# Performance work log

Hardware: AMD Instinct MI355X
Metric: run time of the kernel (lower is better)

The kernel has to match this reference:

```python
import jax, jax.numpy as jnp
import numpy as np

B, S, E, H = 2, 4096, 512, 8
DK = E // H


def setup_inputs() -> dict:
    k = jax.random.key(0)
    ks = jax.random.split(k, 11)
    sc = 0.02
    return {
        "query": jax.random.normal(ks[0], (B, S, E), jnp.float32),
        "key_in": jax.random.normal(ks[1], (B, S, E), jnp.float32),
        "value": jax.random.normal(ks[2], (B, S, E), jnp.float32),
        "Wq": jax.random.normal(ks[3], (E, E), jnp.float32) * sc,
        "bq": jax.random.normal(ks[4], (E,), jnp.float32) * sc,
        "Wk": jax.random.normal(ks[5], (E, E), jnp.float32) * sc,
        "bk": jax.random.normal(ks[6], (E,), jnp.float32) * sc,
        "Wv": jax.random.normal(ks[7], (E, E), jnp.float32) * sc,
        "bv": jax.random.normal(ks[8], (E,), jnp.float32) * sc,
        "Wo": jax.random.normal(ks[9], (E, E), jnp.float32) * sc,
        "bo": jax.random.normal(ks[10], (E,), jnp.float32) * sc,
    }


def reference(query, key_in, value, Wq, bq, Wk, bk, Wv, bv, Wo, bo):
    b, s, _ = query.shape
    # Linear projections
    q = query @ Wq + bq
    k = key_in @ Wk + bk
    v = value @ Wv + bv
    # [b, s, H, dk] -> [b, H, s, dk]
    q = q.reshape(b, s, H, DK).transpose(0, 2, 1, 3)
    k = k.reshape(b, s, H, DK).transpose(0, 2, 1, 3)
    v = v.reshape(b, s, H, DK).transpose(0, 2, 1, 3)
    # NOTE: source bug — softmax over UNSCALED scores (1/sqrt scaling in the
    # original is applied to a dead variable after softmax). Reproduce faithfully.
    scores = jnp.einsum("bhqd,bhkd->bhqk", q, k)  # [b,H,s,s] — O(N^2) materialized
    weights = jax.nn.softmax(scores.astype(jnp.float32), axis=-1)
    attn = jnp.einsum("bhqk,bhkd->bhqd", weights, v)
    # [b,H,s,dk] -> [b,s,E]
    concat = attn.transpose(0, 2, 1, 3).reshape(b, s, E)
    return concat @ Wo + bo
```

## Files before the change

kernel.cpp:

```cpp
#include <hip/hip_runtime.h>
#include <hip/hip_bf16.h>

#define B_  2
#define S_  4096
#define E_  512
#define H_  8
#define DK_ 64
#define M_  8192

typedef float f32x4  __attribute__((ext_vector_type(4)));
typedef float f32x16 __attribute__((ext_vector_type(16)));
typedef short s16x8  __attribute__((ext_vector_type(8)));
typedef short s16x4  __attribute__((ext_vector_type(4)));

static __device__ __forceinline__ short f2bf(float x) {
  __hip_bfloat16 h = __float2bfloat16(x);
  return __builtin_bit_cast(short, h);
}

static __device__ __forceinline__ f32x4 mfma32(s16x8 a, s16x8 b, f32x4 c) {
  return __builtin_amdgcn_mfma_f32_16x16x32_bf16(a, b, c, 0, 0, 0);
}

static __device__ __forceinline__ f32x16 mfma3232(s16x8 a, s16x8 b, f32x16 c) {
  return __builtin_amdgcn_mfma_f32_32x32x16_bf16(a, b, c, 0, 0, 0);
}

static __device__ __forceinline__ float fastexp2(float x) {
#if __has_builtin(__builtin_amdgcn_exp2f)
  return __builtin_amdgcn_exp2f(x);
#else
  return __expf(x * 0.69314718056f);
#endif
}

static __device__ __forceinline__ void gload_lds16(const void* g, void* l) {
  __builtin_amdgcn_global_load_lds(
      (const __attribute__((address_space(1))) unsigned int*)g,
      (__attribute__((address_space(3))) unsigned int*)l, 16, 0, 0);
}

__global__ __launch_bounds__(256) void conv_wT_all(
    const float* __restrict__ Wq, const float* __restrict__ Wk,
    const float* __restrict__ Wv, const float* __restrict__ Wo,
    short* __restrict__ Wt) {
  const float* W = (blockIdx.y == 0) ? Wq
                   : ((blockIdx.y == 1) ? Wk : ((blockIdx.y == 2) ? Wv : Wo));
  short* o = Wt + (size_t)blockIdx.y * (E_ * E_);
  int idx = blockIdx.x * 256 + threadIdx.x;
  int j = idx >> 9, k = idx & 511;
  o[idx] = f2bf(W[(size_t)k * E_ + j]);
}

static __device__ __forceinline__ void gemm_core_512(
    const short* __restrict__ A, const short* __restrict__ Bt,
    short* As, short* Bs, int tm, int tn, f32x4 acc[4][4]) {
  const int tid = threadIdx.x;
  const int wave = tid >> 6, lane = tid & 63;
  const int c = lane & 15, g = lane >> 4;
  int fOff[2];
#pragma unroll
  for (int r = 0; r < 2; ++r) {
    const int f = wave * 2 + r;
    fOff[r] = ((f >> 2) * 64 + (f & 3) * 16 + c) * 512 + g * 8;
  }
  auto stg = [&](int p, int b) {
#pragma unroll
    for (int r = 0; r < 2; ++r) {
      const int f = wave * 2 + r;
      gload_lds16(A + (size_t)tm * 512 + p * 32 + fOff[r],
                  (char*)As + b * 8192 + f * 1024);
      gload_lds16(Bt + (size_t)tn * 512 + p * 32 + fOff[r],
                  (char*)Bs + b * 8192 + f * 1024);
    }
  };
  stg(0, 0);
  __syncthreads();
  for (int p = 0; p < 16; ++p) {
    if (p + 1 < 16) stg(p + 1, (p + 1) & 1);
    const short* Ac = As + (p & 1) * 4096;
    const short* Bc = Bs + (p & 1) * 4096;
    s16x8 af[4], bfr[4];
#pragma unroll
    for (int i = 0; i < 4; ++i)
      af[i] = *(const s16x8*)(Ac + ((wave >> 1) * 4 + i) * 512 + lane * 8);
#pragma unroll
    for (int j = 0; j < 4; ++j)
      bfr[j] = *(const s16x8*)(Bc + ((wave & 1) * 4 + j) * 512 + lane * 8);
#pragma unroll
    for (int i = 0; i < 4; ++i)
#pragma unroll
      for (int j = 0; j < 4; ++j)
        acc[i][j] = mfma32(af[i], bfr[j], acc[i][j]);
    __syncthreads();
  }
}

static __device__ __forceinline__ void gemm_core_f32A(
    const float* __restrict__ A, const short* __restrict__ Bt,
    short* As, short* Bs, int tm, int tn, f32x4 acc[4][4]) {
  const int tid = threadIdx.x;
  const int wave = tid >> 6, lane = tid & 63;
  const int c = lane & 15, g = lane >> 4;
  int fOff[2];
#pragma unroll
  for (int r = 0; r < 2; ++r) {
    const int f = wave * 2 + r;
    fOff[r] = ((f >> 2) * 64 + (f & 3) * 16 + c) * 512 + g * 8;
  }
  auto stgB = [&](int p, int b) {
#pragma unroll
    for (int r = 0; r < 2; ++r)
      gload_lds16(Bt + (size_t)tn * 512 + p * 32 + fOff[r],
                  (char*)Bs + b * 8192 + (wave * 2 + r) * 1024);
  };
  float4 a0[2], a1[2];
  auto ldA = [&](int p) {
#pragma unroll
    for (int r = 0; r < 2; ++r) {
      const float* ap = A + (size_t)tm * 512 + p * 32 + fOff[r];
      a0[r] = *(const float4*)ap;
      a1[r] = *(const float4*)(ap + 4);
    }
  };
  auto wrA = [&](int b) {
#pragma unroll
    for (int r = 0; r < 2; ++r) {
      s16x8 w;
      w[0] = f2bf(a0[r].x); w[1] = f2bf(a0[r].y);
      w[2] = f2bf(a0[r].z); w[3] = f2bf(a0[r].w);
      w[4] = f2bf(a1[r].x); w[5] = f2bf(a1[r].y);
      w[6] = f2bf(a1[r].z); w[7] = f2bf(a1[r].w);
      *(s16x8*)((char*)As + b * 8192 + (wave * 2 + r) * 1024 + lane * 16) = w;
    }
  };
  ldA(0); stgB(0, 0); wrA(0);
  __syncthreads();
  for (int p = 0; p < 16; ++p) {
    if (p + 1 < 16) { ldA(p + 1); stgB(p + 1, (p + 1) & 1); }
    const short* Ac = As + (p & 1) * 4096;
    const short* Bc = Bs + (p & 1) * 4096;
    s16x8 af[4], bfr[4];
#pragma unroll
    for (int i = 0; i < 4; ++i)
      af[i] = *(const s16x8*)(Ac + ((wave >> 1) * 4 + i) * 512 + lane * 8);
#pragma unroll
    for (int j = 0; j < 4; ++j)
      bfr[j] = *(const s16x8*)(Bc + ((wave & 1) * 4 + j) * 512 + lane * 8);
#pragma unroll
    for (int i = 0; i < 4; ++i)
#pragma unroll
      for (int j = 0; j < 4; ++j)
        acc[i][j] = mfma32(af[i], bfr[j], acc[i][j]);
    if (p + 1 < 16) wrA((p + 1) & 1);
    __syncthreads();
  }
}

__global__ __launch_bounds__(256) void gemm_qkv(
    const float* __restrict__ Xq, const float* __restrict__ Xk,
    const float* __restrict__ Xv, const short* __restrict__ Wt,
    const float* __restrict__ bq, const float* __restrict__ bk,
    const float* __restrict__ bv,
    short* __restrict__ Qo, short* __restrict__ Ko, short* __restrict__ Vto) {
  __shared__ __align__(16) short As[2 * 4096];
  __shared__ __align__(16) short Bs[2 * 4096];
  const int z = blockIdx.z;
  const float* A = (z == 0) ? Xq : ((z == 1) ? Xk : Xv);
  const short* Bt = Wt + z * (E_ * E_);
  const float* bias = (z == 0) ? bq : ((z == 1) ? bk : bv);
  const int tm = blockIdx.x * 128, tn = blockIdx.y * 128;
  f32x4 acc[4][4] = {};
  gemm_core_f32A(A, Bt, As, Bs, tm, tn, acc);

  const int tid = threadIdx.x;
  const int wave = tid >> 6, lane = tid & 63;
  const int wm = (wave >> 1) * 64, wn = (wave & 1) * 64;
  const int c = lane & 15, g = lane >> 4;
#pragma unroll
  for (int i = 0; i < 4; ++i) {
#pragma unroll
    for (int j = 0; j < 4; ++j) {
      const int gc = tn + wn + j * 16 + c;
      const float bb = bias[gc];
      const int h = gc >> 6, dk = gc & 63;
      if (z == 2) {
        const int gr0 = tm + wm + i * 16 + g * 4;
        const int b = gr0 >> 12, s0 = gr0 & 4095;
        s16x4 v4;
#pragma unroll
        for (int r = 0; r < 4; ++r) v4[r] = f2bf(acc[i][j][r] + bb);
        *(s16x4*)&Vto[(size_t)((b * H_ + h) * DK_ + dk) * S_ + s0] = v4;
      } else {
#pragma unroll
        for (int r = 0; r < 4; ++r) {
          const int gr = tm + wm + i * 16 + g * 4 + r;
          const int b = gr >> 12, s = gr & 4095;
          float v = acc[i][j][r] + bb;
          if (z == 0) v *= 1.44269504f;
          const short hv = f2bf(v);
          if (z == 1)
            Ko[(size_t)((b * H_ + h) * S_ + s) * DK_ + dk] = hv;
          else
            Qo[(size_t)((b * H_ + h) * S_ + s) * DK_ + dk] = hv;
        }
      }
    }
  }
}

__global__ __launch_bounds__(256) void gemm_out(
    const short* __restrict__ AO, const short* __restrict__ Wot,
    const float* __restrict__ bo, float* __restrict__ out) {
  __shared__ __align__(16) short As[2 * 4096];
  __shared__ __align__(16) short Bs[2 * 4096];
  const int tm = blockIdx.x * 128, tn = blockIdx.y * 128;
  f32x4 acc[4][4] = {};
  gemm_core_512(AO, Wot, As, Bs, tm, tn, acc);

  const int tid = threadIdx.x;
  const int wave = tid >> 6, lane = tid & 63;
  const int wm = (wave >> 1) * 64, wn = (wave & 1) * 64;
  const int c = lane & 15, g = lane >> 4;
#pragma unroll
  for (int i = 0; i < 4; ++i) {
#pragma unroll
    for (int j = 0; j < 4; ++j) {
      const int gc = tn + wn + j * 16 + c;
      const float bb = bo[gc];
#pragma unroll
      for (int r = 0; r < 4; ++r) {
        const int gr = tm + wm + i * 16 + g * 4 + r;
        out[(size_t)gr * E_ + gc] = acc[i][j][r] + bb;
      }
    }
  }
}

__global__ __launch_bounds__(512, 2) void attn_fwd(
    const short* __restrict__ Q, const short* __restrict__ K,
    const short* __restrict__ Vt, short* __restrict__ O) {
  __shared__ __align__(16) char lds[98304];
  const int tid = threadIdx.x;
  const int wave = tid >> 6, lane = tid & 63;
  const int g = wave >> 1, kh = wave & 1;
  const int qi = lane & 31, hi = lane >> 5;
  const int bh = blockIdx.y;
  const int b = bh >> 3, h = bh & 7;
  const int q0 = blockIdx.x * 256 + g * 64;
  const short* Qp = Q + (size_t)bh * S_ * DK_;
  const short* Kp = K + (size_t)bh * S_ * DK_;
  const short* Vp = Vt + (size_t)bh * DK_ * S_;

  s16x8 qfL[4], qfH[4];
#pragma unroll
  for (int s = 0; s < 4; ++s) {
    qfL[s] = *(const s16x8*)(Qp + (size_t)(q0 + qi) * DK_ + s * 16 + hi * 8);
    qfH[s] = *(const s16x8*)(Qp + (size_t)(q0 + 32 + qi) * DK_ + s * 16 + hi * 8);
  }

  f32x16 o00 = {}, o01 = {}, o10 = {}, o11 = {};
  float lsL = 0.f, lsH = 0.f;

  int kOff, vOff;
  {
    const int j = wave;
    const int row = (j >> 2) * 32 + qi;
    const int srow = (row & 32) | ((row & 8) << 1) | ((row & 4) << 1) |
                     ((row & 16) >> 2) | (row & 3);
    kOff = srow * DK_ + (j & 3) * 16 + hi * 8;
    vOff = ((j >> 2) * 32 + qi) * S_ + ((j >> 1) & 1) * 32 +
           (j & 1) * 16 + hi * 8;
  }

  auto stage = [&](int kt) {
    gload_lds16(Kp + (size_t)kt * 64 * DK_ + kOff,
                lds + (kt % 6) * 8192 + wave * 1024);
    gload_lds16(Vp + (size_t)kt * 64 + vOff,
                lds + 49152 + (kt % 6) * 8192 + wave * 1024);
  };

  auto bar4 = [&]() {
    asm volatile("s_waitcnt vmcnt(4) lgkmcnt(0)" ::: "memory");
    __builtin_amdgcn_s_barrier();
  };
  auto bar0 = [&]() {
    asm volatile("s_waitcnt vmcnt(0) lgkmcnt(0)" ::: "memory");
    __builtin_amdgcn_s_barrier();
  };

  const int lbK = kh * 4096 + (lane << 4);

  auto qk = [&](int t, f32x16& sL, f32x16& sH) {
    const char* Kc = lds + (t % 6) * 8192 + lbK;
    f32x16 a = {}, c = {};
    __builtin_amdgcn_s_setprio(1);
#pragma unroll
    for (int s = 0; s < 4; ++s) {
      s16x8 ka = *(const s16x8*)(Kc + s * 1024);
      a = mfma3232(ka, qfL[s], a);
      c = mfma3232(ka, qfH[s], c);
    }
    __builtin_amdgcn_s_setprio(0);
    sL = a; sH = c;
  };

  auto softpv = [&](const f32x16& sL, const f32x16& sH, int t) {
    const char* Vc = lds + 49152 + (t % 6) * 8192 + kh * 2048 + (lane << 4);
    float pL[16], pH[16];
#pragma unroll
    for (int r = 0; r < 16; ++r) { pL[r] = fastexp2(sL[r]); pH[r] = fastexp2(sH[r]); }
    float aL = 0.f, aH = 0.f;
#pragma unroll
    for (int r = 0; r < 16; ++r) { aL += pL[r]; aH += pH[r]; }
    lsL += aL; lsH += aH;
    s16x8 pbL[2], pbH[2];
#pragma unroll
    for (int ks = 0; ks < 2; ++ks)
#pragma unroll
      for (int j = 0; j < 8; ++j) {
        const int r = (j & 3) | (ks << 2) | ((j >> 2) << 3);
        pbL[ks][j] = f2bf(pL[r]);
        pbH[ks][j] = f2bf(pH[r]);
      }
    __builtin_amdgcn_s_setprio(1);
#pragma unroll
    for (int ks = 0; ks < 2; ++ks) {
      s16x8 va0 = *(const s16x8*)(Vc + ks * 1024);
      s16x8 va1 = *(const s16x8*)(Vc + 4096 + ks * 1024);
      o00 = mfma3232(va0, pbL[ks], o00);
      o01 = mfma3232(va0, pbH[ks], o01);
      o10 = mfma3232(va1, pbL[ks], o10);
      o11 = mfma3232(va1, pbH[ks], o11);
    }
    __builtin_amdgcn_s_setprio(0);
  };

  const int NT = S_ / 64;
  f32x16 sA0, sA1, sB0, sB1;

  stage(0); stage(1); stage(2); stage(3);
  bar4();

  for (int t = 0; t < NT; t += 2) {
    if (t + 4 < NT) { stage(t + 4); stage(t + 5); bar4(); } else bar0();
    qk(t, sA0, sA1);
    qk(t + 1, sB0, sB1);
    softpv(sA0, sA1, t);
    softpv(sB0, sB1, t + 1);
  }

  lsL += __shfl_xor(lsL, 32);
  lsH += __shfl_xor(lsH, 32);

  float* mrg = (float*)lds;
  const int mi = (g * 64 + lane) * 36;
  __syncthreads();
  if (kh) {
#pragma unroll
    for (int r = 0; r < 4; ++r) {
      *(f32x4*)(mrg + mi + r * 4) =
          f32x4{o00[r * 4], o00[r * 4 + 1], o00[r * 4 + 2], o00[r * 4 + 3]};
      *(f32x4*)(mrg + mi + 16 + r * 4) =
          f32x4{o01[r * 4], o01[r * 4 + 1], o01[r * 4 + 2], o01[r * 4 + 3]};
    }
    mrg[mi + 32] = lsL;
    mrg[mi + 33] = lsH;
  }
  __syncthreads();
  float rlL = 0.f, rlH = 0.f;
  if (!kh) {
#pragma unroll
    for (int r = 0; r < 16; ++r) {
      o00[r] += mrg[mi + r];
      o01[r] += mrg[mi + 16 + r];
    }
    rlL = 1.f / (lsL + mrg[mi + 32]);
    rlH = 1.f / (lsH + mrg[mi + 33]);
  }
  __syncthreads();
  if (kh) {
#pragma unroll
    for (int r = 0; r < 4; ++r) {
      *(f32x4*)(mrg + mi + r * 4) =
          f32x4{o10[r * 4], o10[r * 4 + 1], o10[r * 4 + 2], o10[r * 4 + 3]};
      *(f32x4*)(mrg + mi + 16 + r * 4) =
          f32x4{o11[r * 4], o11[r * 4 + 1], o11[r * 4 + 2], o11[r * 4 + 3]};
    }
  }
  __syncthreads();
  if (!kh) {
#pragma unroll
    for (int r = 0; r < 16; ++r) {
      o10[r] += mrg[mi + r];
      o11[r] += mrg[mi + 16 + r];
    }
    short* OpL = O + ((size_t)(b * S_ + q0 + qi)) * E_ + h * DK_;
    short* OpH = O + ((size_t)(b * S_ + q0 + 32 + qi)) * E_ + h * DK_;
#pragma unroll
    for (int rr = 0; rr < 4; ++rr) {
      s16x4 vL0, vL1, vH0, vH1;
#pragma unroll
      for (int e = 0; e < 4; ++e) {
        vL0[e] = f2bf(o00[rr * 4 + e] * rlL);
        vL1[e] = f2bf(o10[rr * 4 + e] * rlL);
        vH0[e] = f2bf(o01[rr * 4 + e] * rlH);
        vH1[e] = f2bf(o11[rr * 4 + e] * rlH);
      }
      *(s16x4*)(OpL + rr * 8 + hi * 4) = vL0;
      *(s16x4*)(OpL + 32 + rr * 8 + hi * 4) = vL1;
      *(s16x4*)(OpH + rr * 8 + hi * 4) = vH0;
      *(s16x4*)(OpH + 32 + rr * 8 + hi * 4) = vH1;
    }
  }
}

extern "C" void kernel_launch(void* const* d_in, const int* in_sizes, int n_in,
                              void* d_out, int out_size, void* d_ws, size_t ws_size,
                              hipStream_t stream) {
  const float* query  = (const float*)d_in[0];
  const float* key_in = (const float*)d_in[1];
  const float* value  = (const float*)d_in[2];
  const float* Wq = (const float*)d_in[3];
  const float* bq = (const float*)d_in[4];
  const float* Wk = (const float*)d_in[5];
  const float* bk = (const float*)d_in[6];
  const float* Wv = (const float*)d_in[7];
  const float* bv = (const float*)d_in[8];
  const float* Wo = (const float*)d_in[9];
  const float* bo = (const float*)d_in[10];
  float* out = (float*)d_out;

  const size_t NA = (size_t)M_ * E_;
  short* ws  = (short*)d_ws;
  short* Wt  = ws;
  short* Wot = Wt + 3 * E_ * E_;
  short* Qb  = Wt + 4 * E_ * E_;
  short* Kb  = Qb + NA;
  short* Vtb = Kb + NA;
  short* AO  = Vtb + NA;

  conv_wT_all<<<dim3(E_ * E_ / 256, 4), 256, 0, stream>>>(Wq, Wk, Wv, Wo, Wt);

  gemm_qkv<<<dim3(M_ / 128, E_ / 128, 3), 256, 0, stream>>>(
      query, key_in, value, Wt, bq, bk, bv, Qb, Kb, Vtb);
  attn_fwd<<<dim3(S_ / 256, B_ * H_), 512, 0, stream>>>(Qb, Kb, Vtb, AO);
  gemm_out<<<dim3(M_ / 128, E_ / 128), 256, 0, stream>>>(AO, Wot, bo, out);
}
```

Before: 144.7 us.

## Split attention KV tiles across wave pairs with 128-query blocks and smaller LDS ring

Attention blocks now cover 128 queries instead of 256, and each 64-query group uses four waves. Those waves split the work both by K/V half and by even/odd KV tile, then merge partial outputs and row sums through LDS at the end. The LDS ring drops from six to four stages (64 KB), and launch bounds are raised to allow more blocks per CU. This doubles the grid and is meant to raise occupancy, at the cost of a full barrier per tile pair, less prefetch depth and a three-way merge epilogue.

```diff
diff --git a/kernel.cpp b/kernel.cpp
--- a/kernel.cpp
+++ b/kernel.cpp
@@ -237,17 +237,17 @@
   }
 }
 
-__global__ __launch_bounds__(512, 2) void attn_fwd(
+__global__ __launch_bounds__(512, 4) void attn_fwd(
     const short* __restrict__ Q, const short* __restrict__ K,
     const short* __restrict__ Vt, short* __restrict__ O) {
-  __shared__ __align__(16) char lds[98304];
+  __shared__ __align__(16) char lds[65536];
   const int tid = threadIdx.x;
   const int wave = tid >> 6, lane = tid & 63;
-  const int g = wave >> 1, kh = wave & 1;
+  const int qg = wave >> 2, kh = (wave >> 1) & 1, ts = wave & 1;
   const int qi = lane & 31, hi = lane >> 5;
   const int bh = blockIdx.y;
   const int b = bh >> 3, h = bh & 7;
-  const int q0 = blockIdx.x * 256 + g * 64;
+  const int q0 = blockIdx.x * 128 + qg * 64;
   const short* Qp = Q + (size_t)bh * S_ * DK_;
   const short* Kp = K + (size_t)bh * S_ * DK_;
   const short* Vp = Vt + (size_t)bh * DK_ * S_;
@@ -275,16 +275,12 @@
 
   auto stage = [&](int kt) {
     gload_lds16(Kp + (size_t)kt * 64 * DK_ + kOff,
-                lds + (kt % 6) * 8192 + wave * 1024);
+                lds + (kt & 3) * 8192 + wave * 1024);
     gload_lds16(Vp + (size_t)kt * 64 + vOff,
-                lds + 49152 + (kt % 6) * 8192 + wave * 1024);
-  };
-
-  auto bar4 = [&]() {
-    asm volatile("s_waitcnt vmcnt(4) lgkmcnt(0)" ::: "memory");
-    __builtin_amdgcn_s_barrier();
-  };
-  auto bar0 = [&]() {
+                lds + 32768 + (kt & 3) * 8192 + wave * 1024);
+  };
+
+  auto barD = [&]() {
     asm volatile("s_waitcnt vmcnt(0) lgkmcnt(0)" ::: "memory");
     __builtin_amdgcn_s_barrier();
   };
@@ -292,7 +288,7 @@
   const int lbK = kh * 4096 + (lane << 4);
 
   auto qk = [&](int t, f32x16& sL, f32x16& sH) {
-    const char* Kc = lds + (t % 6) * 8192 + lbK;
+    const char* Kc = lds + (t & 3) * 8192 + lbK;
     f32x16 a = {}, c = {};
     __builtin_amdgcn_s_setprio(1);
 #pragma unroll
@@ -306,7 +302,7 @@
   };
 
   auto softpv = [&](const f32x16& sL, const f32x16& sH, int t) {
-    const char* Vc = lds + 49152 + (t % 6) * 8192 + kh * 2048 + (lane << 4);
+    const char* Vc = lds + 32768 + (t & 3) * 8192 + kh * 2048 + (lane << 4);
     float pL[16], pH[16];
 #pragma unroll
     for (int r = 0; r < 16; ++r) { pL[r] = fastexp2(sL[r]); pH[r] = fastexp2(sH[r]); }
@@ -337,63 +333,75 @@
   };
 
   const int NT = S_ / 64;
-  f32x16 sA0, sA1, sB0, sB1;
-
-  stage(0); stage(1); stage(2); stage(3);
-  bar4();
-
-  for (int t = 0; t < NT; t += 2) {
-    if (t + 4 < NT) { stage(t + 4); stage(t + 5); bar4(); } else bar0();
+  f32x16 sA0, sA1;
+
+  stage(0); stage(1);
+  barD();
+  stage(2); stage(3);
+
+  for (int t2 = 0; t2 < NT; t2 += 2) {
+    const int t = t2 + ts;
     qk(t, sA0, sA1);
-    qk(t + 1, sB0, sB1);
     softpv(sA0, sA1, t);
-    softpv(sB0, sB1, t + 1);
+    barD();
+    if (t2 + 4 < NT) { stage(t2 + 4); stage(t2 + 5); }
   }
 
   lsL += __shfl_xor(lsL, 32);
   lsH += __shfl_xor(lsH, 32);
 
   float* mrg = (float*)lds;
-  const int mi = (g * 64 + lane) * 36;
-  __syncthreads();
-  if (kh) {
+  const int widx = kh * 2 + ts;
+  const int miW = ((qg * 3 + (widx - 1)) * 64 + lane) * 36;
+  __syncthreads();
+  if (widx) {
 #pragma unroll
     for (int r = 0; r < 4; ++r) {
-      *(f32x4*)(mrg + mi + r * 4) =
+      *(f32x4*)(mrg + miW + r * 4) =
           f32x4{o00[r * 4], o00[r * 4 + 1], o00[r * 4 + 2], o00[r * 4 + 3]};
-      *(f32x4*)(mrg + mi + 16 + r * 4) =
+      *(f32x4*)(mrg + miW + 16 + r * 4) =
           f32x4{o01[r * 4], o01[r * 4 + 1], o01[r * 4 + 2], o01[r * 4 + 3]};
     }
-    mrg[mi + 32] = lsL;
-    mrg[mi + 33] = lsH;
+    mrg[miW + 32] = lsL;
+    mrg[miW + 33] = lsH;
   }
   __syncthreads();
   float rlL = 0.f, rlH = 0.f;
-  if (!kh) {
-#pragma unroll
-    for (int r = 0; r < 16; ++r) {
-      o00[r] += mrg[mi + r];
-      o01[r] += mrg[mi + 16 + r];
-    }
-    rlL = 1.f / (lsL + mrg[mi + 32]);
-    rlH = 1.f / (lsH + mrg[mi + 33]);
-  }
-  __syncthreads();
-  if (kh) {
+  if (!widx) {
+#pragma unroll
+    for (int w2 = 0; w2 < 3; ++w2) {
+      const int mi2 = ((qg * 3 + w2) * 64 + lane) * 36;
+#pragma unroll
+      for (int r = 0; r < 16; ++r) {
+        o00[r] += mrg[mi2 + r];
+        o01[r] += mrg[mi2 + 16 + r];
+      }
+      lsL += mrg[mi2 + 32];
+      lsH += mrg[mi2 + 33];
+    }
+    rlL = 1.f / lsL;
+    rlH = 1.f / lsH;
+  }
+  __syncthreads();
+  if (widx) {
 #pragma unroll
     for (int r = 0; r < 4; ++r) {
-      *(f32x4*)(mrg + mi + r * 4) =
+      *(f32x4*)(mrg + miW + r * 4) =
           f32x4{o10[r * 4], o10[r * 4 + 1], o10[r * 4 + 2], o10[r * 4 + 3]};
-      *(f32x4*)(mrg + mi + 16 + r * 4) =
+      *(f32x4*)(mrg + miW + 16 + r * 4) =
           f32x4{o11[r * 4], o11[r * 4 + 1], o11[r * 4 + 2], o11[r * 4 + 3]};
     }
   }
   __syncthreads();
-  if (!kh) {
-#pragma unroll
-    for (int r = 0; r < 16; ++r) {
-      o10[r] += mrg[mi + r];
-      o11[r] += mrg[mi + 16 + r];
+  if (!widx) {
+#pragma unroll
+    for (int w2 = 0; w2 < 3; ++w2) {
+      const int mi2 = ((qg * 3 + w2) * 64 + lane) * 36;
+#pragma unroll
+      for (int r = 0; r < 16; ++r) {
+        o10[r] += mrg[mi2 + r];
+        o11[r] += mrg[mi2 + 16 + r];
+      }
     }
     short* OpL = O + ((size_t)(b * S_ + q0 + qi)) * E_ + h * DK_;
     short* OpH = O + ((size_t)(b * S_ + q0 + 32 + qi)) * E_ + h * DK_;
@@ -444,6 +452,6 @@
 
   gemm_qkv<<<dim3(M_ / 128, E_ / 128, 3), 256, 0, stream>>>(
       query, key_in, value, Wt, bq, bk, bv, Qb, Kb, Vtb);
-  attn_fwd<<<dim3(S_ / 256, B_ * H_), 512, 0, stream>>>(Qb, Kb, Vtb, AO);
+  attn_fwd<<<dim3(S_ / 128, B_ * H_), 512, 0, stream>>>(Qb, Kb, Vtb, AO);
   gemm_out<<<dim3(M_ / 128, E_ / 128), 256, 0, stream>>>(AO, Wot, bo, out);
 }
```

New measurement: 252.4 us. 74.5% more time.

## Compute softmax row sums via MFMA with ones vector and restructure prefetch barrier

Applied to the files above, without the earlier changes.

Replaces the scalar per-lane accumulation of exponentials and the cross-half shuffle with extra MFMA instructions that multiply the bf16 probabilities by a ones vector, so the denominator is built on the matrix cores. The denominator now sums the bf16-rounded probabilities, which matches the values actually fed into the PV product. The loop schedule also changes: instead of issuing the next two tile loads and waiting with vmcnt(4) before compute, it computes first, then does a full vmcnt(0) barrier, then issues the next loads. This may reduce how much load latency is overlapped with compute.

```diff
diff --git a/kernel.cpp b/kernel.cpp
--- a/kernel.cpp
+++ b/kernel.cpp
@@ -260,7 +260,10 @@
   }
 
   f32x16 o00 = {}, o01 = {}, o10 = {}, o11 = {};
-  float lsL = 0.f, lsH = 0.f;
+  f32x16 laccL = {}, laccH = {};
+  s16x8 ones;
+#pragma unroll
+  for (int e = 0; e < 8; ++e) ones[e] = (short)0x3F80;
 
   int kOff, vOff;
   {
@@ -280,11 +283,7 @@
                 lds + 49152 + (kt % 6) * 8192 + wave * 1024);
   };
 
-  auto bar4 = [&]() {
-    asm volatile("s_waitcnt vmcnt(4) lgkmcnt(0)" ::: "memory");
-    __builtin_amdgcn_s_barrier();
-  };
-  auto bar0 = [&]() {
+  auto barD = [&]() {
     asm volatile("s_waitcnt vmcnt(0) lgkmcnt(0)" ::: "memory");
     __builtin_amdgcn_s_barrier();
   };
@@ -310,10 +309,6 @@
     float pL[16], pH[16];
 #pragma unroll
     for (int r = 0; r < 16; ++r) { pL[r] = fastexp2(sL[r]); pH[r] = fastexp2(sH[r]); }
-    float aL = 0.f, aH = 0.f;
-#pragma unroll
-    for (int r = 0; r < 16; ++r) { aL += pL[r]; aH += pH[r]; }
-    lsL += aL; lsH += aH;
     s16x8 pbL[2], pbH[2];
 #pragma unroll
     for (int ks = 0; ks < 2; ++ks)
@@ -332,6 +327,8 @@
       o01 = mfma3232(va0, pbH[ks], o01);
       o10 = mfma3232(va1, pbL[ks], o10);
       o11 = mfma3232(va1, pbH[ks], o11);
+      laccL = mfma3232(ones, pbL[ks], laccL);
+      laccH = mfma3232(ones, pbH[ks], laccH);
     }
     __builtin_amdgcn_s_setprio(0);
   };
@@ -340,18 +337,18 @@
   f32x16 sA0, sA1, sB0, sB1;
 
   stage(0); stage(1); stage(2); stage(3);
-  bar4();
+  barD();
 
   for (int t = 0; t < NT; t += 2) {
-    if (t + 4 < NT) { stage(t + 4); stage(t + 5); bar4(); } else bar0();
     qk(t, sA0, sA1);
     qk(t + 1, sB0, sB1);
     softpv(sA0, sA1, t);
     softpv(sB0, sB1, t + 1);
-  }
-
-  lsL += __shfl_xor(lsL, 32);
-  lsH += __shfl_xor(lsH, 32);
+    barD();
+    if (t + 4 < NT) { stage(t + 4); stage(t + 5); }
+  }
+
+  const float lsL = laccL[0], lsH = laccH[0];
 
   float* mrg = (float*)lds;
   const int mi = (g * 64 + lane) * 36;
@@ -370,13 +367,16 @@
   __syncthreads();
   float rlL = 0.f, rlH = 0.f;
   if (!kh) {
+    float dL = lsL, dH = lsH;
 #pragma unroll
     for (int r = 0; r < 16; ++r) {
       o00[r] += mrg[mi + r];
       o01[r] += mrg[mi + 16 + r];
     }
-    rlL = 1.f / (lsL + mrg[mi + 32]);
-    rlH = 1.f / (lsH + mrg[mi + 33]);
+    dL += mrg[mi + 32];
+    dH += mrg[mi + 33];
+    rlL = 1.f / dL;
+    rlH = 1.f / dH;
   }
   __syncthreads();
   if (kh) {
```

Result: slower. 148.7 us (+2.8%).
